# Performance work log

Measured on AMD Instinct MI355X. Metric: run time of the kernel, lower is better.

## Reference

```python
import jax, jax.numpy as jnp
import numpy as np

B, T, DIM, H = 4, 1024, 2048, 16
HD = DIM // H  # head_dim = 128


def _rope_tables(t, hd, theta=10000.0):
    freqs = 1.0 / (theta ** (np.arange(0, hd, 2, dtype=np.float32) / hd))  # [hd/2]
    ang = np.outer(np.arange(t, dtype=np.float32), freqs)  # [T, hd/2]
    return jnp.asarray(np.cos(ang)), jnp.asarray(np.sin(ang))


def setup_inputs() -> dict:
    key = jax.random.key(0)
    ks = jax.random.split(key, 5)
    x = jax.random.normal(ks[0], (B, T, DIM), dtype=jnp.float32)
    s = 1.0 / np.sqrt(DIM)
    wq = jax.random.normal(ks[1], (DIM, DIM), dtype=jnp.float32) * s
    wk = jax.random.normal(ks[2], (DIM, DIM), dtype=jnp.float32) * s
    wv = jax.random.normal(ks[3], (DIM, DIM), dtype=jnp.float32) * s
    wo = jax.random.normal(ks[4], (DIM, DIM), dtype=jnp.float32) * s
    freqs_cos, freqs_sin = _rope_tables(T, HD)
    return {"x": x, "freqs_cos": freqs_cos, "freqs_sin": freqs_sin,
            "wq": wq, "wk": wk, "wv": wv, "wo": wo}


def _apply_rope(t, cos, sin):
    # t: [B,T,H,HD]; cos/sin: [T,HD/2]. Adjacent feature pairs form complex numbers.
    tr = t.reshape(*t.shape[:-1], HD // 2, 2)
    te, to = tr[..., 0], tr[..., 1]
    c = cos[None, :, None, :]
    s = sin[None, :, None, :]
    oe = te * c - to * s
    oo = te * s + to * c
    return jnp.stack([oe, oo], axis=-1).reshape(t.shape)


def reference(x, freqs_cos, freqs_sin, wq, wk, wv, wo):
    # Linear layers: y = x @ W^T (torch nn.Linear convention)
    q = (x @ wq.T).reshape(B, T, H, HD)
    k = (x @ wk.T).reshape(B, T, H, HD)
    v = (x @ wv.T).reshape(B, T, H, HD)
    q = _apply_rope(q, freqs_cos, freqs_sin)
    k = _apply_rope(k, freqs_cos, freqs_sin)
    scale = 1.0 / jnp.sqrt(jnp.float32(HD))
    # non-causal SDPA (no mask in original call)
    scores = jnp.einsum('bqhd,bkhd->bhqk', q, k) * scale
    attn = jax.nn.softmax(scores, axis=-1)
    out = jnp.einsum('bhqk,bkhd->bqhd', attn, v).reshape(B, T, DIM)
    return out @ wo.T
```

## Files before the change

### kernel.cpp

```cpp
#include <hip/hip_runtime.h>
#include <stdint.h>

#define BB 4
#define TT 1024
#define DIM 2048
#define NH 16
#define HD 128
#define MR 4096
#define QKVS (3 * DIM)

typedef __attribute__((ext_vector_type(4))) float    f32x4;
typedef __attribute__((ext_vector_type(8))) uint16_t u16x8;
typedef __attribute__((ext_vector_type(4))) uint16_t u16x4;
typedef __attribute__((ext_vector_type(4))) short    s16x4;
typedef __attribute__((ext_vector_type(8))) __bf16   bf16x8;

static __device__ __forceinline__ uint16_t f2bf(float f) {
  uint32_t u = __builtin_bit_cast(uint32_t, f);
  u += 0x7fffu + ((u >> 16) & 1u);
  return (uint16_t)(u >> 16);
}
static __device__ __forceinline__ float bf2f(uint16_t b) {
  uint32_t u = ((uint32_t)b) << 16;
  return __builtin_bit_cast(float, u);
}

static __device__ __forceinline__ f32x4 mfma16(u16x8 a, u16x8 b, f32x4 c) {
  return __builtin_amdgcn_mfma_f32_16x16x32_bf16(
      __builtin_bit_cast(bf16x8, a), __builtin_bit_cast(bf16x8, b), c, 0, 0, 0);
}

static __device__ __forceinline__ void load_lds_16B(const void* g, void* l) {
  __builtin_amdgcn_global_load_lds(
      (const __attribute__((address_space(1))) void*)g,
      (__attribute__((address_space(3))) void*)l, 16, 0, 0);
}

#if defined(__has_builtin) && __has_builtin(__builtin_amdgcn_ds_read_tr16_b64_v4i16)
#define TR_BUILTIN 1
#else
#define TR_BUILTIN 0
#endif
static __device__ __forceinline__ u16x4 tr16_nw(const uint16_t* base, int byteoff) {
  __attribute__((address_space(3))) char* ap =
      (__attribute__((address_space(3))) char*)(void*)base + byteoff;
#if TR_BUILTIN
  s16x4 r = __builtin_amdgcn_ds_read_tr16_b64_v4i16(
      (__attribute__((address_space(3))) s16x4*)ap);
  return __builtin_bit_cast(u16x4, r);
#else
  u16x4 d;
  uint32_t a32 = (uint32_t)(uintptr_t)ap;
  asm volatile("ds_read_b64_tr_b16 %0, %1" : "=&v"(d) : "v"(a32));
  return d;
#endif
}
static __device__ __forceinline__ void tr_fence() {
#if !TR_BUILTIN
  asm volatile("s_waitcnt lgkmcnt(0)" ::: "memory");
  __builtin_amdgcn_sched_barrier(0);
#endif
}

__global__ __launch_bounds__(256) void cast_f32_bf16(const float* __restrict__ in,
                                                     uint16_t* __restrict__ out, int n4) {
  int i = blockIdx.x * 256 + threadIdx.x;
  if (i >= n4) return;
  f32x4 v = ((const f32x4*)in)[i];
  u16x4 o;
  o[0] = f2bf(v[0]); o[1] = f2bf(v[1]); o[2] = f2bf(v[2]); o[3] = f2bf(v[3]);
  ((u16x4*)out)[i] = o;
}

__global__ __launch_bounds__(256) void cast4_f32_bf16(const float* __restrict__ s0,
                                                      const float* __restrict__ s1,
                                                      const float* __restrict__ s2,
                                                      const float* __restrict__ s3,
                                                      uint16_t* __restrict__ out) {
  const int per = 4194304 / 4;
  int i = blockIdx.x * 256 + threadIdx.x;
  const int sel = i / per;
  const float* src = (sel == 0) ? s0 : (sel == 1) ? s1 : (sel == 2) ? s2 : s3;
  int j = i - sel * per;
  f32x4 v = ((const f32x4*)src)[j];
  u16x4 o;
  o[0] = f2bf(v[0]); o[1] = f2bf(v[1]); o[2] = f2bf(v[2]); o[3] = f2bf(v[3]);
  ((u16x4*)out)[i] = o;
}

template <int MODE>
__global__ __launch_bounds__(256) void gemm_m97(const uint16_t* __restrict__ A,
                                                const uint16_t* __restrict__ Bt,
                                                float* __restrict__ Cf,
                                                uint16_t* __restrict__ Cb,
                                                const float* __restrict__ cosT,
                                                const float* __restrict__ sinT,
                                                int M, int N, int K) {
  __shared__ __attribute__((aligned(16))) uint16_t As[128][64];
  __shared__ __attribute__((aligned(16))) uint16_t Bs[128][64];
  const int tid  = threadIdx.x;
  const int lane = tid & 63;
  const int wave = tid >> 6;
  const int lrow = lane & 15;
  const int lgrp = lane >> 4;
  const int wr   = (wave >> 1) * 64;
  const int wc   = (wave & 1) * 64;

  const int nbx = N >> 7, nby = M >> 7;
  const int nwg = nbx * nby;
  const int wg  = ((int)blockIdx.x & 7) * (nwg >> 3) + ((int)blockIdx.x >> 3);
  const long bRow = (long)(wg / nbx) << 7;
  const long bCol = (long)(wg % nbx) << 7;

  const f32x4 fz = {0.f, 0.f, 0.f, 0.f};
  f32x4 acc[4][4];
#pragma unroll
  for (int m = 0; m < 4; ++m)
#pragma unroll
    for (int n = 0; n < 4; ++n) acc[m][n] = fz;

  const int nkt = K >> 6;
  for (int kt = 0; kt < nkt; ++kt) {
    const long kb = (long)kt << 6;
    __syncthreads();
#pragma unroll
    for (int i = 0; i < 4; ++i) {
      const int L   = (i * 256 + tid) * 16;
      const int row = L >> 7;
      const int gc  = (((L >> 4) & 7) ^ (row & 7)) * 8;
      load_lds_16B(A  + (bRow + row) * (long)K + kb + gc, (char*)&As[0][0] + L);
      load_lds_16B(Bt + (bCol + row) * (long)K + kb + gc, (char*)&Bs[0][0] + L);
    }
    __syncthreads();

#pragma unroll
    for (int kk = 0; kk < 2; ++kk) {
      u16x8 af[4], bf[4];
#pragma unroll
      for (int m = 0; m < 4; ++m) {
        const int row = wr + m * 16 + lrow;
        const int ch  = (kk * 4 + lgrp) ^ (row & 7);
        af[m] = *(const u16x8*)((const char*)&As[0][0] + row * 128 + ch * 16);
      }
#pragma unroll
      for (int n = 0; n < 4; ++n) {
        const int row = wc + n * 16 + lrow;
        const int ch  = (kk * 4 + lgrp) ^ (row & 7);
        bf[n] = *(const u16x8*)((const char*)&Bs[0][0] + row * 128 + ch * 16);
      }
      __builtin_amdgcn_s_setprio(1);
#pragma unroll
      for (int m = 0; m < 4; ++m)
#pragma unroll
        for (int n = 0; n < 4; ++n) acc[m][n] = mfma16(af[m], bf[n], acc[m][n]);
      __builtin_amdgcn_s_setprio(0);
    }
  }

  const bool doRope = (MODE == 2) && (bCol < 2 * DIM);
  const bool isQ    = (MODE == 2) && (bCol < DIM);
  const float qscale = isQ ? 0.08838834764831845f : 1.0f;
#pragma unroll
  for (int m = 0; m < 4; ++m)
#pragma unroll
    for (int n = 0; n < 4; ++n) {
      const long grow0 = bRow + wr + m * 16 + lgrp * 4;
      const long gcol  = bCol + wc + n * 16 + lrow;
      if (doRope) {
        const int  fi  = ((int)gcol >> 1) & 63;
        const bool odd = (gcol & 1) != 0;
#pragma unroll
        for (int r = 0; r < 4; ++r) {
          const long grow = grow0 + r;
          const int  ttt  = (int)grow & (TT - 1);
          float v = acc[m][n][r];
          float p = __shfl_xor(v, 1, 64);
          float cc = cosT[ttt * 64 + fi];
          float ss = sinT[ttt * 64 + fi];
          float o  = odd ? (p * ss + v * cc) : (v * cc - p * ss);
          Cb[grow * (long)N + gcol] = f2bf(o * qscale);
        }
      } else {
#pragma unroll
        for (int r = 0; r < 4; ++r) {
          const long idx = (grow0 + r) * (long)N + gcol;
          if (MODE == 1) Cf[idx] = acc[m][n][r];
          else           Cb[idx] = f2bf(acc[m][n][r]);
        }
      }
    }
}

__global__ __launch_bounds__(256) void attn_fwd(const uint16_t* __restrict__ Q,
                                                const uint16_t* __restrict__ K,
                                                const uint16_t* __restrict__ V,
                                                uint16_t* __restrict__ O) {
  __shared__ __attribute__((aligned(16))) uint16_t Ks[64 * 128];
  __shared__ __attribute__((aligned(16))) uint16_t Vs[64 * 128];
  __shared__ __attribute__((aligned(16))) uint16_t PsT[4][64 * 16];
  const int tid  = threadIdx.x;
  const int lane = tid & 63;
  const int wave = tid >> 6;
  const int lrow = lane & 15;
  const int lgrp = lane >> 4;
  const int b  = blockIdx.x >> 4;
  const int h  = blockIdx.x & 15;
  const int qt = blockIdx.y;
  const long colBase = (long)h * HD;
  const long rs = QKVS;
  const long os = DIM;
  const long qrow0 = (long)b * TT + qt * 64 + wave * 16;

  u16x8 qf[4];
#pragma unroll
  for (int kkk = 0; kkk < 4; ++kkk)
    qf[kkk] = *(const u16x8*)(Q + (qrow0 + lrow) * rs + colBase + kkk * 32 + lgrp * 8);

  const f32x4 fz = {0.f, 0.f, 0.f, 0.f};
  f32x4 oacc[8];
#pragma unroll
  for (int nf = 0; nf < 8; ++nf) oacc[nf] = fz;
  float mst[4] = {-1e30f, -1e30f, -1e30f, -1e30f};
  float lst[4] = {0.f, 0.f, 0.f, 0.f};

  for (int kt2 = 0; kt2 < TT / 64; ++kt2) {
    const long krow = (long)b * TT + kt2 * 64;
    __syncthreads();
#pragma unroll
    for (int i = 0; i < 4; ++i) {
      const int L = (i * 256 + tid) * 16;
      const int krw = L >> 8;
      const int ksc = ((L >> 4) & 15) ^ (krw & 7);
      load_lds_16B(K + (krow + krw) * rs + colBase + ksc * 8, (char*)Ks + L);
      const int vbl = L >> 11;
      const int vkv = ((L >> 7) & 15) * 4 + ((L >> 5) & 3);
      const int vd  = vbl * 16 + ((L >> 4) & 1) * 8;
      load_lds_16B(V + (krow + vkv) * rs + colBase + vd, (char*)Vs + L);
    }
    __syncthreads();

    f32x4 sacc[4];
#pragma unroll
    for (int n = 0; n < 4; ++n) sacc[n] = fz;
    __builtin_amdgcn_s_setprio(1);
#pragma unroll
    for (int kkk = 0; kkk < 4; ++kkk) {
#pragma unroll
      for (int n = 0; n < 4; ++n) {
        const int row = n * 16 + lrow;
        const int ch  = (kkk * 4 + lgrp) ^ (row & 7);
        u16x8 bfr = *(const u16x8*)((const char*)Ks + row * 256 + ch * 16);
        sacc[n] = mfma16(qf[kkk], bfr, sacc[n]);
      }
    }
    __builtin_amdgcn_s_setprio(0);

    float pm[4];
#pragma unroll
    for (int r = 0; r < 4; ++r)
      pm[r] = fmaxf(fmaxf(sacc[0][r], sacc[1][r]), fmaxf(sacc[2][r], sacc[3][r]));
    bool need = false;
#pragma unroll
    for (int r = 0; r < 4; ++r) need = need || (pm[r] > mst[r] + 8.0f);
    if (__any(need)) {
      float rmax[4];
#pragma unroll
      for (int r = 0; r < 4; ++r) rmax[r] = pm[r];
#pragma unroll
      for (int off = 8; off >= 1; off >>= 1)
#pragma unroll
        for (int r = 0; r < 4; ++r)
          rmax[r] = fmaxf(rmax[r], __shfl_xor(rmax[r], off, 64));
#pragma unroll
      for (int r = 0; r < 4; ++r) {
        float mnew  = fmaxf(mst[r], rmax[r]);
        float alpha = __expf(mst[r] - mnew);
        mst[r] = mnew;
        lst[r] *= alpha;
#pragma unroll
        for (int nf = 0; nf < 8; ++nf) oacc[nf][r] *= alpha;
      }
    }

    const int cb = (lgrp ^ (lrow >> 2)) * 4;
#pragma unroll
    for (int n = 0; n < 4; ++n) {
      float e0 = __expf(sacc[n][0] - mst[0]);
      float e1 = __expf(sacc[n][1] - mst[1]);
      float e2 = __expf(sacc[n][2] - mst[2]);
      float e3 = __expf(sacc[n][3] - mst[3]);
      lst[0] += e0; lst[1] += e1; lst[2] += e2; lst[3] += e3;
      u16x4 pk;
      pk[0] = f2bf(e0); pk[1] = f2bf(e1); pk[2] = f2bf(e2); pk[3] = f2bf(e3);
      *(u16x4*)&PsT[wave][(n * 16 + lrow) * 16 + cb] = pk;
    }

    asm volatile("s_waitcnt lgkmcnt(0)" ::: "memory");

    __builtin_amdgcn_s_setprio(1);
#pragma unroll
    for (int kk2 = 0; kk2 < 2; ++kk2) {
      const int t0 = kk2 * 8 + lgrp * 2;
      u16x4 alo = tr16_nw(&PsT[wave][0],
                          t0 * 128 + ((lrow ^ (t0 & 3)) << 3));
      u16x4 ahi = tr16_nw(&PsT[wave][0],
                          (t0 + 1) * 128 + ((lrow ^ ((t0 + 1) & 3)) << 3));
      u16x4 vlo[8], vhi[8];
#pragma unroll
      for (int nf = 0; nf < 8; ++nf) {
        const int vbase = nf * 2048 + kk2 * 1024 + lgrp * 256 + lrow * 8;
        vlo[nf] = tr16_nw(Vs, vbase);
        vhi[nf] = tr16_nw(Vs, vbase + 128);
      }
      tr_fence();
      u16x8 af;
      af[0] = alo[0]; af[1] = alo[1]; af[2] = alo[2]; af[3] = alo[3];
      af[4] = ahi[0]; af[5] = ahi[1]; af[6] = ahi[2]; af[7] = ahi[3];
#pragma unroll
      for (int nf = 0; nf < 8; ++nf) {
        u16x8 bfr;
        bfr[0] = vlo[nf][0]; bfr[1] = vlo[nf][1];
        bfr[2] = vlo[nf][2]; bfr[3] = vlo[nf][3];
        bfr[4] = vhi[nf][0]; bfr[5] = vhi[nf][1];
        bfr[6] = vhi[nf][2]; bfr[7] = vhi[nf][3];
        oacc[nf] = mfma16(af, bfr, oacc[nf]);
      }
    }
    __builtin_amdgcn_s_setprio(0);
  }

#pragma unroll
  for (int off = 8; off >= 1; off >>= 1)
#pragma unroll
    for (int r = 0; r < 4; ++r) lst[r] += __shfl_xor(lst[r], off, 64);

  float inv[4];
#pragma unroll
  for (int r = 0; r < 4; ++r) inv[r] = 1.0f / lst[r];
#pragma unroll
  for (int nf = 0; nf < 8; ++nf)
#pragma unroll
    for (int r = 0; r < 4; ++r)
      O[(qrow0 + lgrp * 4 + r) * os + colBase + nf * 16 + lrow] =
          f2bf(oacc[nf][r] * inv[r]);
}

extern "C" void kernel_launch(void* const* d_in, const int* in_sizes, int n_in,
                              void* d_out, int out_size, void* d_ws, size_t ws_size,
                              hipStream_t stream) {
  const float* x  = (const float*)d_in[0];
  const float* fc = (const float*)d_in[1];
  const float* fs = (const float*)d_in[2];
  const float* wq = (const float*)d_in[3];
  const float* wk = (const float*)d_in[4];
  const float* wv = (const float*)d_in[5];
  const float* wo = (const float*)d_in[6];
  float* out = (float*)d_out;

  uint16_t* w16  = (uint16_t*)d_ws;
  uint16_t* xb   = w16;
  uint16_t* wqkv = xb + 8388608;
  uint16_t* wob  = wqkv + 12582912;
  uint16_t* qkv  = wob + 4194304;
  uint16_t* ob   = qkv + 25165824;

  cast_f32_bf16<<<8192, 256, 0, stream>>>(x, xb, 8388608 / 4);
  cast4_f32_bf16<<<4 * 4096, 256, 0, stream>>>(wq, wk, wv, wo, wqkv);

  gemm_m97<2><<<(MR / 128) * (QKVS / 128), 256, 0, stream>>>(
      xb, wqkv, nullptr, qkv, fc, fs, MR, QKVS, DIM);

  dim3 ga(BB * NH, TT / 64);
  attn_fwd<<<ga, 256, 0, stream>>>(qkv, qkv + DIM, qkv + 2 * DIM, ob);

  gemm_m97<1><<<(MR / 128) * (DIM / 128), 256, 0, stream>>>(
      ob, wob, out, nullptr, nullptr, nullptr, MR, DIM, DIM);
}
```

Before: 262.2 us.

## Fuse cast kernels and double attention query tile to 128 rows per block

Merges the two f32-to-bf16 cast launches into one kernel covering x and all four weights, removing one launch. The attention kernel now uses 512 threads (8 waves) per block, each block handling 128 query rows, so every K/V tile staged in shared memory is reused by twice as many queries and global K/V traffic is halved. The trade-offs are fewer blocks (512 instead of 1024) for the GPU's compute units and larger per-block shared memory for the P buffers, which may reduce occupancy.

```diff
diff --git a/kernel.cpp b/kernel.cpp
--- a/kernel.cpp
+++ b/kernel.cpp
@@ -62,30 +62,33 @@
 #endif
 }
 
-__global__ __launch_bounds__(256) void cast_f32_bf16(const float* __restrict__ in,
-                                                     uint16_t* __restrict__ out, int n4) {
+__global__ __launch_bounds__(256) void cast_all(const float* __restrict__ x,
+                                                const float* __restrict__ wq,
+                                                const float* __restrict__ wk,
+                                                const float* __restrict__ wv,
+                                                const float* __restrict__ wo,
+                                                uint16_t* __restrict__ xb,
+                                                uint16_t* __restrict__ wall) {
+  const int xn = 8388608 / 4;
+  const int wn = 4194304 / 4;
   int i = blockIdx.x * 256 + threadIdx.x;
-  if (i >= n4) return;
-  f32x4 v = ((const f32x4*)in)[i];
-  u16x4 o;
-  o[0] = f2bf(v[0]); o[1] = f2bf(v[1]); o[2] = f2bf(v[2]); o[3] = f2bf(v[3]);
-  ((u16x4*)out)[i] = o;
-}
-
-__global__ __launch_bounds__(256) void cast4_f32_bf16(const float* __restrict__ s0,
-                                                      const float* __restrict__ s1,
-                                                      const float* __restrict__ s2,
-                                                      const float* __restrict__ s3,
-                                                      uint16_t* __restrict__ out) {
-  const int per = 4194304 / 4;
-  int i = blockIdx.x * 256 + threadIdx.x;
-  const int sel = i / per;
-  const float* src = (sel == 0) ? s0 : (sel == 1) ? s1 : (sel == 2) ? s2 : s3;
-  int j = i - sel * per;
+  const float* src;
+  uint16_t* dst;
+  int j, dj;
+  if (i < xn) {
+    src = x; dst = xb; j = i; dj = i;
+  } else {
+    const int k   = i - xn;
+    const int sel = k / wn;
+    j  = k - sel * wn;
+    dj = k;
+    src = (sel == 0) ? wq : (sel == 1) ? wk : (sel == 2) ? wv : wo;
+    dst = wall;
+  }
   f32x4 v = ((const f32x4*)src)[j];
   u16x4 o;
   o[0] = f2bf(v[0]); o[1] = f2bf(v[1]); o[2] = f2bf(v[2]); o[3] = f2bf(v[3]);
-  ((u16x4*)out)[i] = o;
+  ((u16x4*)dst)[dj] = o;
 }
 
 template <int MODE>
@@ -191,13 +194,13 @@
     }
 }
 
-__global__ __launch_bounds__(256) void attn_fwd(const uint16_t* __restrict__ Q,
+__global__ __launch_bounds__(512) void attn_fwd(const uint16_t* __restrict__ Q,
                                                 const uint16_t* __restrict__ K,
                                                 const uint16_t* __restrict__ V,
                                                 uint16_t* __restrict__ O) {
   __shared__ __attribute__((aligned(16))) uint16_t Ks[64 * 128];
   __shared__ __attribute__((aligned(16))) uint16_t Vs[64 * 128];
-  __shared__ __attribute__((aligned(16))) uint16_t PsT[4][64 * 16];
+  __shared__ __attribute__((aligned(16))) uint16_t PsT[8][64 * 16];
   const int tid  = threadIdx.x;
   const int lane = tid & 63;
   const int wave = tid >> 6;
@@ -209,7 +212,7 @@
   const long colBase = (long)h * HD;
   const long rs = QKVS;
   const long os = DIM;
-  const long qrow0 = (long)b * TT + qt * 64 + wave * 16;
+  const long qrow0 = (long)b * TT + qt * 128 + wave * 16;
 
   u16x8 qf[4];
 #pragma unroll
@@ -227,8 +230,8 @@
     const long krow = (long)b * TT + kt2 * 64;
     __syncthreads();
 #pragma unroll
-    for (int i = 0; i < 4; ++i) {
-      const int L = (i * 256 + tid) * 16;
+    for (int i = 0; i < 2; ++i) {
+      const int L = (i * 512 + tid) * 16;
       const int krw = L >> 8;
       const int ksc = ((L >> 4) & 15) ^ (krw & 7);
       load_lds_16B(K + (krow + krw) * rs + colBase + ksc * 8, (char*)Ks + L);
@@ -364,14 +367,14 @@
   uint16_t* qkv  = wob + 4194304;
   uint16_t* ob   = qkv + 25165824;
 
-  cast_f32_bf16<<<8192, 256, 0, stream>>>(x, xb, 8388608 / 4);
-  cast4_f32_bf16<<<4 * 4096, 256, 0, stream>>>(wq, wk, wv, wo, wqkv);
+  cast_all<<<(8388608 / 4 + 4 * (4194304 / 4)) / 256, 256, 0, stream>>>(
+      x, wq, wk, wv, wo, xb, wqkv);
 
   gemm_m97<2><<<(MR / 128) * (QKVS / 128), 256, 0, stream>>>(
       xb, wqkv, nullptr, qkv, fc, fs, MR, QKVS, DIM);
 
-  dim3 ga(BB * NH, TT / 64);
-  attn_fwd<<<ga, 256, 0, stream>>>(qkv, qkv + DIM, qkv + 2 * DIM, ob);
+  dim3 ga(BB * NH, TT / 128);
+  attn_fwd<<<ga, 512, 0, stream>>>(qkv, qkv + DIM, qkv + 2 * DIM, ob);
 
   gemm_m97<1><<<(MR / 128) * (DIM / 128), 256, 0, stream>>>(
       ob, wob, out, nullptr, nullptr, nullptr, MR, DIM, DIM);
```

Result: faster. 239.5 us (-8.7%).
